# Optimization experiments

Measured on AMD Instinct MI355X. Metric: run time of the kernel, lower is better.

## Reference

```python
import jax, jax.numpy as jnp
import numpy as np

THRESH = 0.5
ALPHA = 1.0
LOG_CLAMP = -100.0  # torch BCELoss clamps log terms at -100


def setup_inputs() -> dict:
    key = jax.random.key(0)
    k1, k2 = jax.random.split(key)
    B, N, C = 2048, 2704, 5
    # predictions: confidences/boxes in (0,1) (post-sigmoid style)
    x = jax.random.uniform(k1, (B, N, C), dtype=jnp.float32, minval=1e-3, maxval=1.0 - 1e-3)
    # labels: conf in [0,1] (~half > 0.5 -> faces), boxes in [0,1]
    y = jax.random.uniform(k2, (B, N, C), dtype=jnp.float32)
    return {"x": x, "y": y}


def _clog(v):
    return jnp.maximum(jnp.log(v), LOG_CLAMP)


def reference(x, y):
    # x, y: [B, N, 5]; channel 0 = confidence, 1:5 = box
    mask = y[..., 0] > THRESH                      # [B, N] face cells
    face_num = jnp.sum(mask).astype(x.dtype)
    bg_num = mask.size - face_num
    scale = 1.0 + 1.0 / face_num

    # MSE over masked boxes, mean over (face_num * 4) elements
    sq = jnp.sum((x[..., 1:5] - y[..., 1:5]) ** 2, axis=-1)   # [B, N]
    diff_box = scale * jnp.sum(jnp.where(mask, sq, 0.0)) / (face_num * 4.0)

    # BCE(pred_conf, label_conf) over face cells, mean
    p = x[..., 0]
    t = y[..., 0]
    bce = -(t * _clog(p) + (1.0 - t) * _clog(1.0 - p))        # [B, N]
    diff_c = scale * jnp.sum(jnp.where(mask, bce, 0.0)) / face_num

    # BCE(pred_conf, 0) over background cells, mean
    bg_bce = -_clog(1.0 - p)                                  # [B, N]
    diff_bg = ALPHA * jnp.sum(jnp.where(mask, 0.0, bg_bce)) / bg_num

    return diff_box + diff_c + diff_bg
```

## Files before the change

kernel.cpp:

```cpp
#include <hip/hip_runtime.h>


#define BLOCK 256
#define TPC 4
#define LOG_CLAMP -100.0f

typedef float nvec4 __attribute__((ext_vector_type(4)));

__device__ __forceinline__ float clogf(float v) {
    return fmaxf(logf(v), LOG_CLAMP);
}

__global__ __launch_bounds__(BLOCK) void mloss_reduce(
    const float* __restrict__ x, const float* __restrict__ y,
    float4* __restrict__ partials, int n_chunks)
{
    const int lane = threadIdx.x & 63;
    const int wv   = threadIdx.x >> 6;

    const nvec4*  gx4 = (const nvec4*)x;
    const float4* gy4 = (const float4*)y;

    float s_sq = 0.0f, s_bce = 0.0f, s_bg = 0.0f, s_cnt = 0.0f;

    for (int c = blockIdx.x; c < n_chunks; c += gridDim.x) {
        int    rr[TPC];
        nvec4  x4[TPC];
        float4 y4[TPC];
        float  yc0[TPC];
        #pragma unroll
        for (int k = 0; k < TPC; ++k) {
            const int g  = (c * TPC + k) * 256 + wv * 64 + lane;
            const int e0 = g * 4;
            const int r  = e0 % 5;
            rr[k] = r;
            x4[k] = __builtin_nontemporal_load(&gx4[g]);
            y4[k] = gy4[g];
            yc0[k] = (lane == 0 && r != 0) ? y[e0 - r] : 0.0f;
        }

        #pragma unroll
        for (int k = 0; k < TPC; ++k) {
            const int    r = rr[k];
            const nvec4  X = x4[k];
            const float4 Y = y4[k];

            const int jc = (5 - r) % 5;
            const float tnext = (jc == 0) ? Y.x : (jc == 1) ? Y.y : (jc == 2) ? Y.z : Y.w;
            const float pconf = (jc == 0) ? X.x : (jc == 1) ? X.y : (jc == 2) ? X.z : X.w;
            const bool  has_conf = (r != 1);

            const float lp  = clogf(pconf);
            const float l1p = clogf(1.0f - pconf);
            const bool  mc  = tnext > 0.5f;
            s_bce += (has_conf && mc)  ? -(tnext * lp + (1.0f - tnext) * l1p) : 0.0f;
            s_bg  += (has_conf && !mc) ? -l1p : 0.0f;
            s_cnt += (has_conf && mc)  ? 1.0f : 0.0f;

            const float outv = (r == 0) ? Y.x : (r == 2) ? Y.w : (r == 3) ? Y.z : Y.y;
            float ycp = __shfl_up(outv, 1, 64);
            if (lane == 0) ycp = yc0[k];
            const float yc = (r == 0) ? Y.x : ycp;

            #define MLOSS_BOX(J, XJ, YJ) do {                                 \
                const int   m  = r + (J);                                     \
                const bool  ic = (m == 0) || (m == 5);                        \
                const float tj = (m >= 5) ? tnext : yc;                       \
                const float d  = (XJ) - (YJ);                                 \
                s_sq += (!ic && tj > 0.5f) ? d * d : 0.0f;                    \
            } while (0)
            MLOSS_BOX(0, X.x, Y.x);
            MLOSS_BOX(1, X.y, Y.y);
            MLOSS_BOX(2, X.z, Y.z);
            MLOSS_BOX(3, X.w, Y.w);
            #undef MLOSS_BOX
        }
    }

    #pragma unroll
    for (int off = 32; off > 0; off >>= 1) {
        s_sq  += __shfl_down(s_sq,  off, 64);
        s_bce += __shfl_down(s_bce, off, 64);
        s_bg  += __shfl_down(s_bg,  off, 64);
        s_cnt += __shfl_down(s_cnt, off, 64);
    }
    __shared__ float4 r_part[BLOCK / 64];
    if (lane == 0) r_part[wv] = make_float4(s_sq, s_bce, s_bg, s_cnt);
    __syncthreads();
    if (threadIdx.x == 0) {
        float4 t0 = r_part[0];
        #pragma unroll
        for (int w = 1; w < BLOCK / 64; ++w) {
            t0.x += r_part[w].x; t0.y += r_part[w].y;
            t0.z += r_part[w].z; t0.w += r_part[w].w;
        }
        partials[blockIdx.x] = t0;
    }
}

#define FBLOCK 1024
__global__ __launch_bounds__(FBLOCK) void mloss_final(
    const float4* __restrict__ partials, int n_parts,
    const float* __restrict__ x, const float* __restrict__ y,
    float* __restrict__ out, long long elem_start, long long n_elems,
    long long n_cells)
{
    double s_sq = 0.0, s_bce = 0.0, s_bg = 0.0, s_cnt = 0.0;
    for (int i = threadIdx.x; i < n_parts; i += FBLOCK) {
        const float4 v = partials[i];
        s_sq += (double)v.x; s_bce += (double)v.y;
        s_bg += (double)v.z; s_cnt += (double)v.w;
    }

    #pragma unroll
    for (int off = 32; off > 0; off >>= 1) {
        s_sq  += __shfl_down(s_sq,  off, 64);
        s_bce += __shfl_down(s_bce, off, 64);
        s_bg  += __shfl_down(s_bg,  off, 64);
        s_cnt += __shfl_down(s_cnt, off, 64);
    }

    __shared__ double r[FBLOCK / 64][4];
    const int wave = threadIdx.x >> 6;
    const int lane = threadIdx.x & 63;
    if (lane == 0) { r[wave][0] = s_sq; r[wave][1] = s_bce; r[wave][2] = s_bg; r[wave][3] = s_cnt; }
    __syncthreads();

    if (threadIdx.x == 0) {
        double t_sq = 0.0, t_bce = 0.0, t_bg = 0.0, face = 0.0;
        #pragma unroll
        for (int w = 0; w < FBLOCK / 64; ++w) {
            t_sq += r[w][0]; t_bce += r[w][1]; t_bg += r[w][2]; face += r[w][3];
        }
        for (long long e = elem_start; e < n_elems; ++e) {
            const long long m  = e % 5;
            const float t_cell = y[e - m];
            const bool  mask   = t_cell > 0.5f;
            if (m == 0) {
                const float p   = x[e];
                const float lp  = clogf(p);
                const float l1p = clogf(1.0f - p);
                if (mask) { t_bce += (double)(-(t_cell * lp + (1.0f - t_cell) * l1p)); face += 1.0; }
                else      { t_bg  += (double)(-l1p); }
            } else if (mask) {
                const float d = x[e] - y[e];
                t_sq += (double)(d * d);
            }
        }
        const double bg    = (double)n_cells - face;
        const double scale = 1.0 + 1.0 / face;
        *out = (float)(scale * t_sq / (face * 4.0) + scale * t_bce / face + t_bg / bg);
    }
}

extern "C" void kernel_launch(void* const* d_in, const int* in_sizes, int n_in,
                              void* d_out, int out_size, void* d_ws, size_t ws_size,
                              hipStream_t stream) {
    const float* x = (const float*)d_in[0];
    const float* y = (const float*)d_in[1];
    float* out = (float*)d_out;
    float4* partials = (float4*)d_ws;

    const long long n_elems  = (long long)in_sizes[0];
    const long long n_cells  = n_elems / 5;
    const long long n_groups = n_elems / 4;
    const long long n_tiles  = n_groups / 256;
    const int       n_chunks = (int)(n_tiles / TPC);
    const long long covered  = (long long)n_chunks * TPC * 256 * 4;

    const int NB = (n_chunks < 2048) ? (n_chunks > 0 ? n_chunks : 1) : 2048;

    if (n_chunks > 0)
        mloss_reduce<<<NB, BLOCK, 0, stream>>>(x, y, partials, n_chunks);
    mloss_final<<<1, FBLOCK, 0, stream>>>(partials, (n_chunks > 0) ? NB : 0,
                                          x, y, out, covered, n_elems, n_cells);
}
```

Before: 228.2 us.

## Double-buffer chunk loads in reduce kernel and halve tiles per chunk

Restructures the grid-stride loop in the reduction kernel into a software-pipelined ping-pong: the next chunk's loads are issued before computing the current chunk, with sched_barrier keeping them apart. TPC drops from 4 to 2 so the two buffers hold about as many registers as before, and launch bounds now request 8 blocks per CU. The aim is to hide global memory latency inside each wave. Chunks get smaller, so there are twice as many loop iterations, and the occupancy hint may cause register spilling.

```diff
diff --git a/kernel.cpp b/kernel.cpp
--- a/kernel.cpp
+++ b/kernel.cpp
@@ -2,7 +2,7 @@
 
 
 #define BLOCK 256
-#define TPC 4
+#define TPC 2
 #define LOG_CLAMP -100.0f
 
 typedef float nvec4 __attribute__((ext_vector_type(4)));
@@ -11,7 +11,73 @@
     return fmaxf(logf(v), LOG_CLAMP);
 }
 
-__global__ __launch_bounds__(BLOCK) void mloss_reduce(
+struct ChunkBuf {
+    nvec4  x4[TPC];
+    float4 y4[TPC];
+    float  yc0[TPC];
+    int    rr[TPC];
+};
+
+__device__ __forceinline__ void load_chunk(
+    int c, int wv, int lane,
+    const nvec4* __restrict__ gx4, const float4* __restrict__ gy4,
+    const float* __restrict__ y, ChunkBuf& b)
+{
+    #pragma unroll
+    for (int k = 0; k < TPC; ++k) {
+        const int g  = (c * TPC + k) * 256 + wv * 64 + lane;
+        const int e0 = g * 4;
+        const int r  = e0 % 5;
+        b.rr[k]  = r;
+        b.x4[k]  = __builtin_nontemporal_load(&gx4[g]);
+        b.y4[k]  = gy4[g];
+        b.yc0[k] = (lane == 0 && r != 0) ? y[e0 - r] : 0.0f;
+    }
+}
+
+__device__ __forceinline__ void compute_chunk(
+    const ChunkBuf& b, int lane,
+    float& s_sq, float& s_bce, float& s_bg, float& s_cnt)
+{
+    #pragma unroll
+    for (int k = 0; k < TPC; ++k) {
+        const int    r = b.rr[k];
+        const nvec4  X = b.x4[k];
+        const float4 Y = b.y4[k];
+
+        const int jc = (5 - r) % 5;
+        const float tnext = (jc == 0) ? Y.x : (jc == 1) ? Y.y : (jc == 2) ? Y.z : Y.w;
+        const float pconf = (jc == 0) ? X.x : (jc == 1) ? X.y : (jc == 2) ? X.z : X.w;
+        const bool  has_conf = (r != 1);
+
+        const float lp  = clogf(pconf);
+        const float l1p = clogf(1.0f - pconf);
+        const bool  mc  = tnext > 0.5f;
+        s_bce += (has_conf && mc)  ? -(tnext * lp + (1.0f - tnext) * l1p) : 0.0f;
+        s_bg  += (has_conf && !mc) ? -l1p : 0.0f;
+        s_cnt += (has_conf && mc)  ? 1.0f : 0.0f;
+
+        const float outv = (r == 0) ? Y.x : (r == 2) ? Y.w : (r == 3) ? Y.z : Y.y;
+        float ycp = __shfl_up(outv, 1, 64);
+        if (lane == 0) ycp = b.yc0[k];
+        const float yc = (r == 0) ? Y.x : ycp;
+
+        #define MLOSS_BOX(J, XJ, YJ) do {                                 \
+            const int   m  = r + (J);                                     \
+            const bool  ic = (m == 0) || (m == 5);                        \
+            const float tj = (m >= 5) ? tnext : yc;                       \
+            const float d  = (XJ) - (YJ);                                 \
+            s_sq += (!ic && tj > 0.5f) ? d * d : 0.0f;                    \
+        } while (0)
+        MLOSS_BOX(0, X.x, Y.x);
+        MLOSS_BOX(1, X.y, Y.y);
+        MLOSS_BOX(2, X.z, Y.z);
+        MLOSS_BOX(3, X.w, Y.w);
+        #undef MLOSS_BOX
+    }
+}
+
+__global__ __launch_bounds__(BLOCK, 8) void mloss_reduce(
     const float* __restrict__ x, const float* __restrict__ y,
     float4* __restrict__ partials, int n_chunks)
 {
@@ -23,57 +89,30 @@
 
     float s_sq = 0.0f, s_bce = 0.0f, s_bg = 0.0f, s_cnt = 0.0f;
 
-    for (int c = blockIdx.x; c < n_chunks; c += gridDim.x) {
-        int    rr[TPC];
-        nvec4  x4[TPC];
-        float4 y4[TPC];
-        float  yc0[TPC];
-        #pragma unroll
-        for (int k = 0; k < TPC; ++k) {
-            const int g  = (c * TPC + k) * 256 + wv * 64 + lane;
-            const int e0 = g * 4;
-            const int r  = e0 % 5;
-            rr[k] = r;
-            x4[k] = __builtin_nontemporal_load(&gx4[g]);
-            y4[k] = gy4[g];
-            yc0[k] = (lane == 0 && r != 0) ? y[e0 - r] : 0.0f;
-        }
-
-        #pragma unroll
-        for (int k = 0; k < TPC; ++k) {
-            const int    r = rr[k];
-            const nvec4  X = x4[k];
-            const float4 Y = y4[k];
-
-            const int jc = (5 - r) % 5;
-            const float tnext = (jc == 0) ? Y.x : (jc == 1) ? Y.y : (jc == 2) ? Y.z : Y.w;
-            const float pconf = (jc == 0) ? X.x : (jc == 1) ? X.y : (jc == 2) ? X.z : X.w;
-            const bool  has_conf = (r != 1);
-
-            const float lp  = clogf(pconf);
-            const float l1p = clogf(1.0f - pconf);
-            const bool  mc  = tnext > 0.5f;
-            s_bce += (has_conf && mc)  ? -(tnext * lp + (1.0f - tnext) * l1p) : 0.0f;
-            s_bg  += (has_conf && !mc) ? -l1p : 0.0f;
-            s_cnt += (has_conf && mc)  ? 1.0f : 0.0f;
-
-            const float outv = (r == 0) ? Y.x : (r == 2) ? Y.w : (r == 3) ? Y.z : Y.y;
-            float ycp = __shfl_up(outv, 1, 64);
-            if (lane == 0) ycp = yc0[k];
-            const float yc = (r == 0) ? Y.x : ycp;
-
-            #define MLOSS_BOX(J, XJ, YJ) do {                                 \
-                const int   m  = r + (J);                                     \
-                const bool  ic = (m == 0) || (m == 5);                        \
-                const float tj = (m >= 5) ? tnext : yc;                       \
-                const float d  = (XJ) - (YJ);                                 \
-                s_sq += (!ic && tj > 0.5f) ? d * d : 0.0f;                    \
-            } while (0)
-            MLOSS_BOX(0, X.x, Y.x);
-            MLOSS_BOX(1, X.y, Y.y);
-            MLOSS_BOX(2, X.z, Y.z);
-            MLOSS_BOX(3, X.w, Y.w);
-            #undef MLOSS_BOX
+    int c = blockIdx.x;
+    const int stride = gridDim.x;
+    if (c < n_chunks) {
+        ChunkBuf A, B;
+        load_chunk(c, wv, lane, gx4, gy4, y, A);
+        c += stride;
+        while (true) {
+            if (c >= n_chunks) {
+                compute_chunk(A, lane, s_sq, s_bce, s_bg, s_cnt);
+                break;
+            }
+            load_chunk(c, wv, lane, gx4, gy4, y, B);
+            __builtin_amdgcn_sched_barrier(0);
+            compute_chunk(A, lane, s_sq, s_bce, s_bg, s_cnt);
+            c += stride;
+
+            if (c >= n_chunks) {
+                compute_chunk(B, lane, s_sq, s_bce, s_bg, s_cnt);
+                break;
+            }
+            load_chunk(c, wv, lane, gx4, gy4, y, A);
+            __builtin_amdgcn_sched_barrier(0);
+            compute_chunk(B, lane, s_sq, s_bce, s_bg, s_cnt);
+            c += stride;
         }
     }
 
```

Result: slower. 237.4 us (+4.0%).

## Stream inputs through per-wave LDS ring with async global_load_lds pipelining

Applied to the files above, without the earlier changes.

Replaces the grid-strided register loads with a per-wave contiguous partition of the input. Each wave prefetches DEPTH slices of x and y directly into LDS using global_load_lds and keeps a software pipeline fenced by vmcnt waits. Because a wave's slices are consecutive, the cell-confidence carry passes between slices through a lane-63 shuffle, which removes the extra scalar load per tile. This aims to keep more memory traffic in flight on a bandwidth-bound reduction. In exchange it adds LDS traffic and a hand-tuned waitcnt that relies on a fixed count of outstanding loads.

```diff
diff --git a/kernel.cpp b/kernel.cpp
--- a/kernel.cpp
+++ b/kernel.cpp
@@ -2,7 +2,8 @@
 
 
 #define BLOCK 256
-#define TPC 4
+#define WPB   (BLOCK / 64)
+#define DEPTH 4
 #define LOG_CLAMP -100.0f
 
 typedef float nvec4 __attribute__((ext_vector_type(4)));
@@ -11,39 +12,49 @@
     return fmaxf(logf(v), LOG_CLAMP);
 }
 
+__device__ __forceinline__ void stage_slice(
+    const nvec4* __restrict__ gx4, const nvec4* __restrict__ gy4,
+    int sg, float* ldsx, int lane)
+{
+    __builtin_amdgcn_global_load_lds(
+        (const __attribute__((address_space(1))) void*)(gx4 + sg + lane),
+        (__attribute__((address_space(3))) void*)ldsx, 16, 0, 0);
+    __builtin_amdgcn_global_load_lds(
+        (const __attribute__((address_space(1))) void*)(gy4 + sg + lane),
+        (__attribute__((address_space(3))) void*)(ldsx + 256), 16, 0, 0);
+}
+
 __global__ __launch_bounds__(BLOCK) void mloss_reduce(
     const float* __restrict__ x, const float* __restrict__ y,
-    float4* __restrict__ partials, int n_chunks)
+    float4* __restrict__ partials, int nsteps_total, int nw)
 {
     const int lane = threadIdx.x & 63;
     const int wv   = threadIdx.x >> 6;
-
-    const nvec4*  gx4 = (const nvec4*)x;
-    const float4* gy4 = (const float4*)y;
+    const int wid  = blockIdx.x * WPB + wv;
+
+    __shared__ float lds[WPB][DEPTH][512];
+
+    const nvec4* gx4 = (const nvec4*)x;
+    const nvec4* gy4 = (const nvec4*)y;
 
     float s_sq = 0.0f, s_bce = 0.0f, s_bg = 0.0f, s_cnt = 0.0f;
 
-    for (int c = blockIdx.x; c < n_chunks; c += gridDim.x) {
-        int    rr[TPC];
-        nvec4  x4[TPC];
-        float4 y4[TPC];
-        float  yc0[TPC];
-        #pragma unroll
-        for (int k = 0; k < TPC; ++k) {
-            const int g  = (c * TPC + k) * 256 + wv * 64 + lane;
-            const int e0 = g * 4;
-            const int r  = e0 % 5;
-            rr[k] = r;
-            x4[k] = __builtin_nontemporal_load(&gx4[g]);
-            y4[k] = gy4[g];
-            yc0[k] = (lane == 0 && r != 0) ? y[e0 - r] : 0.0f;
-        }
-
-        #pragma unroll
-        for (int k = 0; k < TPC; ++k) {
-            const int    r = rr[k];
-            const nvec4  X = x4[k];
-            const float4 Y = y4[k];
+    const int S = nsteps_total / nw;
+    const int R = nsteps_total % nw;
+    const int steps = (wid < nw) ? (S + (wid < R ? 1 : 0)) : 0;
+    const int start = wid * S + (wid < R ? wid : R);
+    const int wgb   = start * 64;
+
+    if (steps > 0) {
+        const int e00 = wgb * 4;
+        float carry = y[e00 - (e00 % 5)];
+
+        int r = (e00 + lane * 4) % 5;
+
+        auto consume = [&](int t) {
+            const float* Lx = &lds[wv][t & (DEPTH - 1)][0];
+            const nvec4 X = *(const nvec4*)(Lx + lane * 4);
+            const nvec4 Y = *(const nvec4*)(Lx + 256 + lane * 4);
 
             const int jc = (5 - r) % 5;
             const float tnext = (jc == 0) ? Y.x : (jc == 1) ? Y.y : (jc == 2) ? Y.z : Y.w;
@@ -59,7 +70,8 @@
 
             const float outv = (r == 0) ? Y.x : (r == 2) ? Y.w : (r == 3) ? Y.z : Y.y;
             float ycp = __shfl_up(outv, 1, 64);
-            if (lane == 0) ycp = yc0[k];
+            if (lane == 0) ycp = carry;
+            carry = __shfl(outv, 63, 64);
             const float yc = (r == 0) ? Y.x : ycp;
 
             #define MLOSS_BOX(J, XJ, YJ) do {                                 \
@@ -74,7 +86,27 @@
             MLOSS_BOX(2, X.z, Y.z);
             MLOSS_BOX(3, X.w, Y.w);
             #undef MLOSS_BOX
-        }
+
+            r = (r == 4) ? 0 : r + 1;
+        };
+
+        #pragma unroll
+        for (int j = 0; j < DEPTH; ++j)
+            if (j < steps)
+                stage_slice(gx4, gy4, wgb + j * 64, &lds[wv][j][0], lane);
+
+        int t = 0;
+        for (; t + DEPTH < steps; ++t) {
+            asm volatile("s_waitcnt vmcnt(6)" ::: "memory");
+            __builtin_amdgcn_sched_barrier(0);
+            consume(t);
+            __builtin_amdgcn_sched_barrier(0);
+            stage_slice(gx4, gy4, wgb + (t + DEPTH) * 64,
+                        &lds[wv][t & (DEPTH - 1)][0], lane);
+        }
+        asm volatile("s_waitcnt vmcnt(0)" ::: "memory");
+        __builtin_amdgcn_sched_barrier(0);
+        for (; t < steps; ++t) consume(t);
     }
 
     #pragma unroll
@@ -84,13 +116,13 @@
         s_bg  += __shfl_down(s_bg,  off, 64);
         s_cnt += __shfl_down(s_cnt, off, 64);
     }
-    __shared__ float4 r_part[BLOCK / 64];
+    __shared__ float4 r_part[WPB];
     if (lane == 0) r_part[wv] = make_float4(s_sq, s_bce, s_bg, s_cnt);
     __syncthreads();
     if (threadIdx.x == 0) {
         float4 t0 = r_part[0];
         #pragma unroll
-        for (int w = 1; w < BLOCK / 64; ++w) {
+        for (int w = 1; w < WPB; ++w) {
             t0.x += r_part[w].x; t0.y += r_part[w].y;
             t0.z += r_part[w].z; t0.w += r_part[w].w;
         }
@@ -161,17 +193,18 @@
     float* out = (float*)d_out;
     float4* partials = (float4*)d_ws;
 
-    const long long n_elems  = (long long)in_sizes[0];
-    const long long n_cells  = n_elems / 5;
-    const long long n_groups = n_elems / 4;
-    const long long n_tiles  = n_groups / 256;
-    const int       n_chunks = (int)(n_tiles / TPC);
-    const long long covered  = (long long)n_chunks * TPC * 256 * 4;
-
-    const int NB = (n_chunks < 2048) ? (n_chunks > 0 ? n_chunks : 1) : 2048;
-
-    if (n_chunks > 0)
-        mloss_reduce<<<NB, BLOCK, 0, stream>>>(x, y, partials, n_chunks);
-    mloss_final<<<1, FBLOCK, 0, stream>>>(partials, (n_chunks > 0) ? NB : 0,
+    const long long n_elems      = (long long)in_sizes[0];
+    const long long n_cells      = n_elems / 5;
+    const long long n_groups     = n_elems / 4;
+    const int       nsteps_total = (int)(n_groups / 64);
+    const long long covered      = (long long)nsteps_total * 256;
+
+    int nw = 5120;
+    if (nsteps_total < nw) nw = (nsteps_total > 0) ? nsteps_total : 1;
+    const int NB = (nw + WPB - 1) / WPB;
+
+    if (nsteps_total > 0)
+        mloss_reduce<<<NB, BLOCK, 0, stream>>>(x, y, partials, nsteps_total, nw);
+    mloss_final<<<1, FBLOCK, 0, stream>>>(partials, (nsteps_total > 0) ? NB : 0,
                                           x, y, out, covered, n_elems, n_cells);
 }
```

Result: slower. 251.2 us (+10.1%).
